# Optimization experiments

Measured on AMD Instinct MI355X. Metric: run time of the kernel, lower is better.

Reference implementation:

```python
import jax, jax.numpy as jnp
import numpy as np


def _ktk(kz):
    t = np.arange(kz, dtype=np.float64)
    A = np.ones((kz * kz, 3))
    A[:, 0] = np.repeat(t, kz)   # temp.repeat(kz)
    A[:, 1] = np.tile(t, kz)     # temp.repeat(kz).reshape(kz,kz).T.reshape(-1)
    k = A @ np.linalg.inv(A.T @ A) @ A.T - np.eye(kz * kz)
    return jnp.asarray(k.T @ k, dtype=jnp.float32)


def _patches(g, kz):
    # g: (b, H, W) -> (b, kz*kz, h, w) with patch index q = a*kz + c for offset (a, c),
    # matching torch conv2d weight flattening (valid padding, stride 1).
    return jax.lax.conv_general_dilated_patches(
        g[:, None, :, :], filter_shape=(kz, kz), window_strides=(1, 1),
        padding='VALID')


def _affine_loss(flow, kz, KTK):
    # flow: (b, 2, H, W), H == W (original code uses arange(w) for both axes)
    W = flow.shape[-1]
    coord = jnp.arange(W, dtype=flow.dtype)
    gx = flow[:, 0] + coord[None, None, :]   # x = column index grid
    gy = flow[:, 1] + coord[None, :, None]   # y = row index grid

    def chan_loss(g):
        P = _patches(g, kz)  # (b, kz^2, h, w)
        # conv2d(grid, KTK rows) -> R_q = sum_r KTK[q,r] P_r ;
        # BlockExtractor(f=kz//2) + LocalAttnReshape + mul + avg_pool(kz)*kz^2 + mean
        # == mean over (b,h,w) of p^T KTK p
        return jnp.mean(jnp.einsum('bqhw,qr,brhw->bhw', P, KTK, P))

    return chan_loss(gx) + chan_loss(gy)


def setup_inputs() -> dict:
    key = jax.random.key(0)
    k0, k1 = jax.random.split(key)
    flow0 = jax.random.normal(k0, (32, 2, 128, 128), dtype=jnp.float32)
    flow1 = jax.random.normal(k1, (32, 2, 256, 256), dtype=jnp.float32)
    return {"flow0": flow0, "flow1": flow1}


def reference(flow0, flow1):
    # kz_dic = {"2": 5, "3": 3}; layers = sorted(keys, reverse=True) = ["3", "2"]
    loss = _affine_loss(flow0, 3, _ktk(3))
    loss = loss + _affine_loss(flow1, 5, _ktk(5))
    return loss
```

## Files before the change

### kernel.cpp

```cpp
#include <hip/hip_runtime.h>


template<int KZ, int W, int STRIP>
__device__ __forceinline__ float patch_strip_acc(const float* __restrict__ flow,
                                                 int nitems, int bid, int nblocks) {
    constexpr int VX     = 2;
    constexpr int Wout   = W - KZ + 1;
    constexpr int XB     = Wout / VX;
    constexpr int NSTRIP = Wout / STRIP;
    constexpr int ROWS   = STRIP + KZ - 1;
    constexpr int NF     = VX + KZ - 1;
    const float m = (KZ - 1) * 0.5f;

    float Ssum = 0.f;
#pragma unroll
    for (int t = 0; t < KZ; ++t) Ssum += (t - m) * (t - m);
    const float invS  = 1.0f / (Ssum * KZ);
    const float invk2 = 1.0f / (KZ * KZ);

    float acc = 0.f;
    for (int item = bid * blockDim.x + threadIdx.x; item < nitems;
         item += nblocks * blockDim.x) {
        int xb = item % XB;
        int t1 = item / XB;
        int ys = (t1 % NSTRIP) * STRIP;
        int bc = t1 / NSTRIP;
        const float* base = flow + (size_t)bc * (W * W) + (size_t)ys * W + xb * VX;

        float rsb[KZ][VX];
        float rssb[KZ][VX];
        float rscb[KZ][VX];
#pragma unroll
        for (int r = 0; r < ROWS; ++r) {
            const float* rowp = base + r * W;
            float v[NF];
            {
                float4 u = *reinterpret_cast<const float4*>(rowp);
                v[0] = u.x; v[1] = u.y; v[2] = u.z; v[3] = u.w;
            }
            if constexpr (NF == 6) {
                float2 u = *reinterpret_cast<const float2*>(rowp + 4);
                v[4] = u.x; v[5] = u.y;
            }
            const int slot = r % KZ;
#pragma unroll
            for (int j = 0; j < VX; ++j) {
                float rs = 0.f, rss = 0.f, rsc = 0.f;
#pragma unroll
                for (int c = 0; c < KZ; ++c) {
                    float p = v[j + c];
                    rs  += p;
                    rss += p * p;
                    rsc += (c - m) * p;
                }
                rsb[slot][j]  = rs;
                rssb[slot][j] = rss;
                rscb[slot][j] = rsc;
            }
            if (r >= KZ - 1) {
                const int y = r - (KZ - 1);
#pragma unroll
                for (int j = 0; j < VX; ++j) {
                    float sum = 0.f, sumsq = 0.f, sa = 0.f, sc = 0.f;
#pragma unroll
                    for (int a = 0; a < KZ; ++a) {
                        const int s = (y + a) % KZ;
                        sum   += rsb[s][j];
                        sumsq += rssb[s][j];
                        sa    += (a - m) * rsb[s][j];
                        sc    += rscb[s][j];
                    }
                    acc += sumsq - sum * sum * invk2 - (sa * sa + sc * sc) * invS;
                }
            }
        }
    }
    return acc;
}

__global__ __launch_bounds__(256, 6) void fused_patch_loss(
        const float* __restrict__ flow0, const float* __restrict__ flow1,
        int nb0, int ni0, int ni1, float s0, float s1,
        float* __restrict__ partial) {
    float acc;
    if ((int)blockIdx.x < nb0) {
        acc = s0 * patch_strip_acc<3, 128, 7>(flow0, ni0, blockIdx.x, nb0);
    } else {
        acc = s1 * patch_strip_acc<5, 256, 9>(flow1, ni1, blockIdx.x - nb0,
                                              gridDim.x - nb0);
    }
    for (int off = 32; off > 0; off >>= 1) acc += __shfl_down(acc, off);
    __shared__ float red[4];
    int lane = threadIdx.x & 63;
    int wid  = threadIdx.x >> 6;
    if (lane == 0) red[wid] = acc;
    __syncthreads();
    if (threadIdx.x == 0)
        partial[blockIdx.x] = red[0] + red[1] + red[2] + red[3];
}

__global__ void final_reduce_kernel(const float* __restrict__ partial, int n,
                                    float* __restrict__ out) {
    float acc = 0.f;
    for (int i = threadIdx.x; i < n; i += blockDim.x) acc += partial[i];
    for (int off = 32; off > 0; off >>= 1) acc += __shfl_down(acc, off);
    __shared__ float red[4];
    int lane = threadIdx.x & 63;
    int wid  = threadIdx.x >> 6;
    if (lane == 0) red[wid] = acc;
    __syncthreads();
    if (threadIdx.x == 0) out[0] = red[0] + red[1] + red[2] + red[3];
}

extern "C" void kernel_launch(void* const* d_in, const int* in_sizes, int n_in,
                              void* d_out, int out_size, void* d_ws, size_t ws_size,
                              hipStream_t stream) {
    const float* flow0 = (const float*)d_in[0];
    const float* flow1 = (const float*)d_in[1];
    float* out = (float*)d_out;
    float* partial = (float*)d_ws;

    const int ni0 = 63 * 18 * 64;
    const int ni1 = 126 * 28 * 64;
    const int nb0 = (ni0 + 255) / 256;
    const int nb1 = ni1 / 256;
    const int nbt = nb0 + nb1;

    const float s0 = 1.0f / (32.0f * 126.0f * 126.0f);
    const float s1 = 1.0f / (32.0f * 252.0f * 252.0f);

    fused_patch_loss<<<nbt, 256, 0, stream>>>(flow0, flow1, nb0, ni0, ni1,
                                              s0, s1, partial);
    final_reduce_kernel<<<1, 256, 0, stream>>>(partial, nbt, out);
}
```

Baseline: 93.17 us.

## Replace final reduce kernel with atomicAdd, shrink KZ=5 strip, use float2 loads

Drops the second reduction kernel and has each block atomically add its partial sum into the output, which is zeroed by a memset beforehand. The aim is to remove a kernel launch and its serialization. The KZ=5 strip height goes from 9 to 7 (36 strips), giving more work items and blocks but more halo row reloads. Row loads become uniform float2 loads instead of float4+float2, and the occupancy hint in launch_bounds is removed; the atomic accumulation makes the summation order nondeterministic.

```diff
diff --git a/kernel.cpp b/kernel.cpp
--- a/kernel.cpp
+++ b/kernel.cpp
@@ -9,7 +9,6 @@
     constexpr int XB     = Wout / VX;
     constexpr int NSTRIP = Wout / STRIP;
     constexpr int ROWS   = STRIP + KZ - 1;
-    constexpr int NF     = VX + KZ - 1;
     const float m = (KZ - 1) * 0.5f;
 
     float Ssum = 0.f;
@@ -33,14 +32,12 @@
 #pragma unroll
         for (int r = 0; r < ROWS; ++r) {
             const float* rowp = base + r * W;
-            float v[NF];
-            {
-                float4 u = *reinterpret_cast<const float4*>(rowp);
-                v[0] = u.x; v[1] = u.y; v[2] = u.z; v[3] = u.w;
-            }
-            if constexpr (NF == 6) {
-                float2 u = *reinterpret_cast<const float2*>(rowp + 4);
-                v[4] = u.x; v[5] = u.y;
+            float v[KZ + 1];
+#pragma unroll
+            for (int q = 0; q < (KZ + 1) / 2; ++q) {
+                float2 u = *reinterpret_cast<const float2*>(rowp + 2 * q);
+                v[2 * q]     = u.x;
+                v[2 * q + 1] = u.y;
             }
             const int slot = r % KZ;
 #pragma unroll
@@ -78,15 +75,15 @@
     return acc;
 }
 
-__global__ __launch_bounds__(256, 6) void fused_patch_loss(
+__global__ __launch_bounds__(256) void fused_patch_loss(
         const float* __restrict__ flow0, const float* __restrict__ flow1,
         int nb0, int ni0, int ni1, float s0, float s1,
-        float* __restrict__ partial) {
+        float* __restrict__ out) {
     float acc;
     if ((int)blockIdx.x < nb0) {
         acc = s0 * patch_strip_acc<3, 128, 7>(flow0, ni0, blockIdx.x, nb0);
     } else {
-        acc = s1 * patch_strip_acc<5, 256, 9>(flow1, ni1, blockIdx.x - nb0,
+        acc = s1 * patch_strip_acc<5, 256, 7>(flow1, ni1, blockIdx.x - nb0,
                                               gridDim.x - nb0);
     }
     for (int off = 32; off > 0; off >>= 1) acc += __shfl_down(acc, off);
@@ -96,20 +93,7 @@
     if (lane == 0) red[wid] = acc;
     __syncthreads();
     if (threadIdx.x == 0)
-        partial[blockIdx.x] = red[0] + red[1] + red[2] + red[3];
-}
-
-__global__ void final_reduce_kernel(const float* __restrict__ partial, int n,
-                                    float* __restrict__ out) {
-    float acc = 0.f;
-    for (int i = threadIdx.x; i < n; i += blockDim.x) acc += partial[i];
-    for (int off = 32; off > 0; off >>= 1) acc += __shfl_down(acc, off);
-    __shared__ float red[4];
-    int lane = threadIdx.x & 63;
-    int wid  = threadIdx.x >> 6;
-    if (lane == 0) red[wid] = acc;
-    __syncthreads();
-    if (threadIdx.x == 0) out[0] = red[0] + red[1] + red[2] + red[3];
+        atomicAdd(out, red[0] + red[1] + red[2] + red[3]);
 }
 
 extern "C" void kernel_launch(void* const* d_in, const int* in_sizes, int n_in,
@@ -118,10 +102,9 @@
     const float* flow0 = (const float*)d_in[0];
     const float* flow1 = (const float*)d_in[1];
     float* out = (float*)d_out;
-    float* partial = (float*)d_ws;
 
     const int ni0 = 63 * 18 * 64;
-    const int ni1 = 126 * 28 * 64;
+    const int ni1 = 126 * 36 * 64;
     const int nb0 = (ni0 + 255) / 256;
     const int nb1 = ni1 / 256;
     const int nbt = nb0 + nb1;
@@ -129,7 +112,7 @@
     const float s0 = 1.0f / (32.0f * 126.0f * 126.0f);
     const float s1 = 1.0f / (32.0f * 252.0f * 252.0f);
 
+    hipMemsetAsync(out, 0, sizeof(float), stream);
     fused_patch_loss<<<nbt, 256, 0, stream>>>(flow0, flow1, nb0, ni0, ni1,
-                                              s0, s1, partial);
-    final_reduce_kernel<<<1, 256, 0, stream>>>(partial, nbt, out);
+                                              s0, s1, out);
 }
```

Result: faster. 86.41 us (-7.3%).
